# Performance work log

Measured on AMD Instinct MI355X. Metric: run time of the kernel, lower is better.

The kernel has to match this reference:

```python
import jax, jax.numpy as jnp
import numpy as np

B, T, C, H = 16, 2048, 192, 64

def setup_inputs() -> dict:
    key = jax.random.key(0)
    k1, k2, k3, k4 = jax.random.split(key, 4)
    x = jax.random.normal(k1, (B, T, C), dtype=jnp.float32)
    Wq = jax.random.normal(k2, (C, H), dtype=jnp.float32) * (C ** -0.5)
    Wk = jax.random.normal(k3, (C, H), dtype=jnp.float32) * (C ** -0.5)
    Wv = jax.random.normal(k4, (C, H), dtype=jnp.float32) * (C ** -0.5)
    return {"x": x, "Wq": Wq, "Wk": Wk, "Wv": Wv}

def reference(x, Wq, Wk, Wv):
    # One head of causal self-attention (dropout in eval mode / identity).
    q = x @ Wq                       # [B, T, H]
    k = x @ Wk                       # [B, T, H]
    v = x @ Wv                       # [B, T, H]
    scale = q.shape[-1] ** -0.5
    wei = jnp.einsum('bth,bsh->bts', q, k) * scale   # [B, T, T]
    t = wei.shape[-1]
    causal = jnp.tril(jnp.ones((t, t), dtype=bool))  # tril mask
    wei = jnp.where(causal, wei, -jnp.inf)
    wei = jax.nn.softmax(wei, axis=-1)
    out = jnp.einsum('bts,bsh->bth', wei, v)         # [B, T, H]
    return out
```

## Files before the change

### kernel.cpp

```cpp
#include <hip/hip_runtime.h>

#define B 16
#define T 2048
#define C 192
#define H 64

typedef __bf16 bf16x8 __attribute__((ext_vector_type(8)));
typedef __bf16 bf16x4 __attribute__((ext_vector_type(4)));
typedef float  f32x4  __attribute__((ext_vector_type(4)));

#define MFMA(a, b, c) __builtin_amdgcn_mfma_f32_16x16x32_bf16(a, b, c, 0, 0, 0)

#define SM_BIAS 24.0f

__global__ __launch_bounds__(512) void qkv_mfma_kernel(
    const float* __restrict__ x,
    const float* __restrict__ Wq, const float* __restrict__ Wk,
    const float* __restrict__ Wv,
    __bf16* __restrict__ qb, __bf16* __restrict__ kb, __bf16* __restrict__ vt)
{
    __shared__ __bf16 Ws[192][200];
    __shared__ __bf16 tile[128][72];

    const int tid  = threadIdx.x;
    const int w    = tid >> 6;
    const int lid  = tid & 15;
    const int quad = (tid & 63) >> 4;
    const int m0   = blockIdx.x * 128 + w * 16;

    #pragma unroll
    for (int i = 0; i < 18; i++) {
        const int p = i * 512 + tid;
        const int m = p / 3072;
        const int r = p - m * 3072;
        const int k = r >> 4;
        const int nc4 = (r & 15) << 2;
        const float* W = (m == 0) ? Wq : (m == 1) ? Wk : Wv;
        const float4 v = *(const float4*)(W + k * H + nc4);
        const int n = m * 64 + nc4;
        Ws[n + 0][k] = (__bf16)v.x;
        Ws[n + 1][k] = (__bf16)v.y;
        Ws[n + 2][k] = (__bf16)v.z;
        Ws[n + 3][k] = (__bf16)v.w;
    }

    const float* xrow = x + (size_t)(m0 + lid) * C + quad * 8;
    bf16x8 af[6];
    #pragma unroll
    for (int kc = 0; kc < 6; kc++) {
        const float4 a0 = *(const float4*)(xrow + kc * 32);
        const float4 a1 = *(const float4*)(xrow + kc * 32 + 4);
        af[kc][0] = (__bf16)a0.x; af[kc][1] = (__bf16)a0.y;
        af[kc][2] = (__bf16)a0.z; af[kc][3] = (__bf16)a0.w;
        af[kc][4] = (__bf16)a1.x; af[kc][5] = (__bf16)a1.y;
        af[kc][6] = (__bf16)a1.z; af[kc][7] = (__bf16)a1.w;
    }
    __syncthreads();

    f32x4 acc[12] = {};
    #pragma unroll
    for (int kc = 0; kc < 6; kc++)
        #pragma unroll
        for (int nt = 0; nt < 12; nt++) {
            const bf16x8 bfr =
                *(const bf16x8*)&Ws[nt * 16 + lid][kc * 32 + quad * 8];
            acc[nt] = MFMA(af[kc], bfr, acc[nt]);
        }

    #pragma unroll
    for (int nt = 0; nt < 8; nt++) {
        const int n = nt * 16 + lid;
        __bf16* dst = (n < 64) ? qb : kb;
        const int col = n & 63;
        const float scale = (n < 64) ? 0.1803368801111204f : 1.0f;
        #pragma unroll
        for (int r = 0; r < 4; r++) {
            const int row = m0 + quad * 4 + r;
            dst[(size_t)row * H + col] = (__bf16)(acc[nt][r] * scale);
        }
    }

    #pragma unroll
    for (int nt = 8; nt < 12; nt++) {
        const int col = (nt - 8) * 16 + lid;
        #pragma unroll
        for (int r = 0; r < 4; r++)
            tile[w * 16 + quad * 4 + r][col] = (__bf16)(acc[nt][r]);
    }
    __syncthreads();

    const int bb = blockIdx.x >> 4;
    const int t0 = (blockIdx.x & 15) << 7;
    #pragma unroll
    for (int it = 0; it < 2; ++it) {
        const int q   = it * 512 + tid;
        const int h   = q >> 4;
        const int tl0 = (q & 15) * 8;
        bf16x8 d;
        #pragma unroll
        for (int j = 0; j < 8; j++) d[j] = tile[tl0 + j][h];
        *(bf16x8*)(vt + ((size_t)(bb * H + h)) * T + t0 + tl0) = d;
    }
}

__global__ __launch_bounds__(512, 4) void attn_kernel(
    const __bf16* __restrict__ qb,
    const __bf16* __restrict__ kb,
    const __bf16* __restrict__ vt,
    float* __restrict__ out)
{
    __shared__ __bf16 Kb[2][2][64][72];
    __shared__ __bf16 Vb[2][2][64][68];

    const int tid  = threadIdx.x;
    const int wv   = tid >> 6;
    const int grp  = wv >> 2;
    const int w    = wv & 3;
    const int lid  = tid & 15;
    const int quad = (tid & 63) >> 4;

    const int half = blockIdx.x >> 8;
    const int rem  = blockIdx.x & 255;
    const int b    = rem & 15;
    const int pr   = rem >> 4;
    const int qt   = half ? pr : (31 - pr);
    const int nch  = qt + 1;
    const int nsteps = (nch + 1) >> 1;
    const size_t bbase = (size_t)b * T;

    const int qX = (qt << 6) + w * 16;

    const __bf16* qr = qb + (bbase + qX + lid) * H + quad * 8;
    const bf16x8 qf0 = *(const bf16x8*)(qr);
    const bf16x8 qf1 = *(const bf16x8*)(qr + 32);

    const __bf16* kgb = kb + bbase * H;
    const __bf16* vgb = vt + (size_t)b * H * T;

    const int ra = tid >> 3, ca = (tid & 7) * 8;

    auto keyof = [&](int i) {
        if (i > nch - 1) i = nch - 1;
        return i << 6;
    };

    bf16x8 kr[2], vr2[2];
    auto prefetch = [&](int s) {
        #pragma unroll
        for (int g = 0; g < 2; g++) {
            const int key0 = keyof(2 * s + g);
            kr[g]  = *(const bf16x8*)(kgb + (size_t)(key0 + ra) * H + ca);
            vr2[g] = *(const bf16x8*)(vgb + (size_t)ra * T + key0 + ca);
        }
    };

    f32x4 O[4] = {};
    float ls = 0.f;

    auto doChunk = [&](int key0, int cur) {
        const __bf16 (*Kc)[72] = Kb[cur][grp];
        const __bf16 (*Vc)[68] = Vb[cur][grp];
        bf16x8 kf[8];
        #pragma unroll
        for (int j = 0; j < 4; j++) {
            kf[2*j]   = *(const bf16x8*)&Kc[j * 16 + lid][quad * 8];
            kf[2*j+1] = *(const bf16x8*)&Kc[j * 16 + lid][32 + quad * 8];
        }
        bf16x8 bv0[4], bv1[4];
        #pragma unroll
        for (int ht = 0; ht < 4; ht++) {
            const __bf16* vr_ = &Vc[ht * 16 + lid][quad * 4];
            ((bf16x4*)&bv0[ht])[0] = *(const bf16x4*)(vr_);
            ((bf16x4*)&bv0[ht])[1] = *(const bf16x4*)(vr_ + 16);
            ((bf16x4*)&bv1[ht])[0] = *(const bf16x4*)(vr_ + 32);
            ((bf16x4*)&bv1[ht])[1] = *(const bf16x4*)(vr_ + 48);
        }
        bf16x8 af0, af1;
        const bool boundary = (key0 + 63 > qX);
        #pragma unroll
        for (int j = 0; j < 4; j++) {
            f32x4 sS = {-SM_BIAS, -SM_BIAS, -SM_BIAS, -SM_BIAS};
            sS = MFMA(kf[2*j], qf0, sS);
            sS = MFMA(kf[2*j+1], qf1, sS);
            if (boundary) {
                #pragma unroll
                for (int r = 0; r < 4; r++)
                    if (key0 + j * 16 + quad * 4 + r > qX + lid) sS[r] = -1e30f;
            }
            #pragma unroll
            for (int r = 0; r < 4; r++) {
                const float p = __builtin_amdgcn_exp2f(sS[r]);
                ls += p;
                if      (j == 0) af0[r]     = (__bf16)p;
                else if (j == 1) af0[4 + r] = (__bf16)p;
                else if (j == 2) af1[r]     = (__bf16)p;
                else             af1[4 + r] = (__bf16)p;
            }
        }
        #pragma unroll
        for (int ht = 0; ht < 4; ht++) {
            O[ht] = MFMA(af0, bv0[ht], O[ht]);
            O[ht] = MFMA(af1, bv1[ht], O[ht]);
        }
    };

    prefetch(0);
    int cur = 0;
    for (int s = 0; s < nsteps; s++) {
        *(bf16x8*)&Kb[cur][0][ra][ca] = kr[0];
        *(bf16x8*)&Kb[cur][1][ra][ca] = kr[1];
        *(bf16x8*)&Vb[cur][0][ra][ca] = vr2[0];
        *(bf16x8*)&Vb[cur][1][ra][ca] = vr2[1];
        __syncthreads();
        if (s + 1 < nsteps) prefetch(s + 1);

        const int i = 2 * s + grp;
        if (i < nch) doChunk(i << 6, cur);
        cur ^= 1;
    }

    __syncthreads();
    float* sO = (float*)&Kb[0][0][0][0];
    float* sL = (float*)&Vb[0][0][0][0];

    float l = ls;
    l += __shfl_xor(l, 16, 64);
    l += __shfl_xor(l, 32, 64);

    if (grp == 1) {
        #pragma unroll
        for (int ht = 0; ht < 4; ht++)
            #pragma unroll
            for (int r = 0; r < 4; r++)
                sO[(w * 16 + quad * 4 + r) * 64 + ht * 16 + lid] = O[ht][r];
        if ((tid & 63) < 16) sL[w * 16 + lid] = l;
    }
    __syncthreads();
    if (grp == 0) {
        l += sL[w * 16 + lid];
        #pragma unroll
        for (int ht = 0; ht < 4; ht++)
            #pragma unroll
            for (int r = 0; r < 4; r++) {
                const float Lr = __shfl(l, quad * 4 + r, 16);
                const float v = O[ht][r]
                    + sO[(w * 16 + quad * 4 + r) * 64 + ht * 16 + lid];
                out[(bbase + qX + quad * 4 + r) * H + ht * 16 + lid] = v / Lr;
            }
    }
}

extern "C" void kernel_launch(void* const* d_in, const int* in_sizes, int n_in,
                              void* d_out, int out_size, void* d_ws, size_t ws_size,
                              hipStream_t stream)
{
    const float* x  = (const float*)d_in[0];
    const float* Wq = (const float*)d_in[1];
    const float* Wk = (const float*)d_in[2];
    const float* Wv = (const float*)d_in[3];

    const size_t BTH = (size_t)B * T * H;
    __bf16* qbuf = (__bf16*)d_ws;
    __bf16* kbuf = qbuf + BTH;
    __bf16* vtb  = kbuf + BTH;
    float* outp = (float*)d_out;

    qkv_mfma_kernel<<<B * T / 128, 512, 0, stream>>>(x, Wq, Wk, Wv,
                                                     qbuf, kbuf, vtb);
    attn_kernel<<<B * T / 128 * 2, 512, 0, stream>>>(qbuf, kbuf, vtb, outp);
}
```

Measured before the change: 101.6 us.

## Pre-pack weights into MFMA fragment layout and split QKV projection across wave groups

Adds a small kernel that converts Wq/Wk/Wv to bf16 once per call and stores them in the exact per-lane MFMA B-fragment order in workspace. The projection kernel then reads weight fragments straight from global memory instead of having every block rebuild a 192x192 bf16 copy in LDS. Each block now covers 64 rows, with two wave groups each computing half of the output columns, which doubles the block count and shrinks LDS use. The cost is an extra kernel launch, and every wave now reads its weight fragments from global or L2 instead of LDS.

Measured after the change: 106.2 us. 1.05x slower.

```diff
diff --git a/kernel.cpp b/kernel.cpp
--- a/kernel.cpp
+++ b/kernel.cpp
@@ -13,36 +13,39 @@
 
 #define SM_BIAS 24.0f
 
-__global__ __launch_bounds__(512) void qkv_mfma_kernel(
+__global__ __launch_bounds__(512) void wtrans_kernel(
+    const float* __restrict__ Wq, const float* __restrict__ Wk,
+    const float* __restrict__ Wv, __bf16* __restrict__ Wf)
+{
+    const int idx  = blockIdx.x * 512 + threadIdx.x;
+    const int ntg  = idx / 384;
+    const int rem  = idx - ntg * 384;
+    const int kc   = rem >> 6;
+    const int lane = rem & 63;
+    const float* Wm = (ntg < 4) ? Wq : (ntg < 8) ? Wk : Wv;
+    const int nl = ((ntg & 3) << 4) + (lane & 15);
+    const int k0 = kc * 32 + (lane >> 4) * 8;
+    bf16x8 d;
+    #pragma unroll
+    for (int j = 0; j < 8; j++) d[j] = (__bf16)Wm[(k0 + j) * H + nl];
+    *(bf16x8*)(Wf + (size_t)idx * 8) = d;
+}
+
+__global__ __launch_bounds__(512, 4) void qkv_mfma_kernel(
     const float* __restrict__ x,
-    const float* __restrict__ Wq, const float* __restrict__ Wk,
-    const float* __restrict__ Wv,
+    const __bf16* __restrict__ Wf,
     __bf16* __restrict__ qb, __bf16* __restrict__ kb, __bf16* __restrict__ vt)
 {
-    __shared__ __bf16 Ws[192][200];
-    __shared__ __bf16 tile[128][72];
+    __shared__ __bf16 tile[64][72];
 
     const int tid  = threadIdx.x;
     const int w    = tid >> 6;
+    const int wg   = w >> 2;
+    const int wr   = w & 3;
+    const int lane = tid & 63;
     const int lid  = tid & 15;
-    const int quad = (tid & 63) >> 4;
-    const int m0   = blockIdx.x * 128 + w * 16;
-
-    #pragma unroll
-    for (int i = 0; i < 18; i++) {
-        const int p = i * 512 + tid;
-        const int m = p / 3072;
-        const int r = p - m * 3072;
-        const int k = r >> 4;
-        const int nc4 = (r & 15) << 2;
-        const float* W = (m == 0) ? Wq : (m == 1) ? Wk : Wv;
-        const float4 v = *(const float4*)(W + k * H + nc4);
-        const int n = m * 64 + nc4;
-        Ws[n + 0][k] = (__bf16)v.x;
-        Ws[n + 1][k] = (__bf16)v.y;
-        Ws[n + 2][k] = (__bf16)v.z;
-        Ws[n + 3][k] = (__bf16)v.w;
-    }
+    const int quad = lane >> 4;
+    const int m0   = blockIdx.x * 64 + wr * 16;
 
     const float* xrow = x + (size_t)(m0 + lid) * C + quad * 8;
     bf16x8 af[6];
@@ -55,47 +58,45 @@
         af[kc][4] = (__bf16)a1.x; af[kc][5] = (__bf16)a1.y;
         af[kc][6] = (__bf16)a1.z; af[kc][7] = (__bf16)a1.w;
     }
+
+    f32x4 acc[6] = {};
+    #pragma unroll
+    for (int kc = 0; kc < 6; kc++)
+        #pragma unroll
+        for (int nt = 0; nt < 6; nt++) {
+            const int ntg = wg * 6 + nt;
+            const bf16x8 bfr = *(const bf16x8*)(
+                Wf + (((size_t)(ntg * 6 + kc)) * 64 + lane) * 8);
+            acc[nt] = MFMA(af[kc], bfr, acc[nt]);
+        }
+
+    #pragma unroll
+    for (int nt = 0; nt < 6; nt++) {
+        const int ntg = wg * 6 + nt;
+        const int n = ntg * 16 + lid;
+        if (ntg < 8) {
+            __bf16* dst = (ntg < 4) ? qb : kb;
+            const int col = n & 63;
+            const float scale = (ntg < 4) ? 0.1803368801111204f : 1.0f;
+            #pragma unroll
+            for (int r = 0; r < 4; r++) {
+                const int row = m0 + quad * 4 + r;
+                dst[(size_t)row * H + col] = (__bf16)(acc[nt][r] * scale);
+            }
+        } else {
+            const int col = n - 128;
+            #pragma unroll
+            for (int r = 0; r < 4; r++)
+                tile[wr * 16 + quad * 4 + r][col] = (__bf16)(acc[nt][r]);
+        }
+    }
     __syncthreads();
 
-    f32x4 acc[12] = {};
-    #pragma unroll
-    for (int kc = 0; kc < 6; kc++)
-        #pragma unroll
-        for (int nt = 0; nt < 12; nt++) {
-            const bf16x8 bfr =
-                *(const bf16x8*)&Ws[nt * 16 + lid][kc * 32 + quad * 8];
-            acc[nt] = MFMA(af[kc], bfr, acc[nt]);
-        }
-
-    #pragma unroll
-    for (int nt = 0; nt < 8; nt++) {
-        const int n = nt * 16 + lid;
-        __bf16* dst = (n < 64) ? qb : kb;
-        const int col = n & 63;
-        const float scale = (n < 64) ? 0.1803368801111204f : 1.0f;
-        #pragma unroll
-        for (int r = 0; r < 4; r++) {
-            const int row = m0 + quad * 4 + r;
-            dst[(size_t)row * H + col] = (__bf16)(acc[nt][r] * scale);
-        }
-    }
-
-    #pragma unroll
-    for (int nt = 8; nt < 12; nt++) {
-        const int col = (nt - 8) * 16 + lid;
-        #pragma unroll
-        for (int r = 0; r < 4; r++)
-            tile[w * 16 + quad * 4 + r][col] = (__bf16)(acc[nt][r]);
-    }
-    __syncthreads();
-
-    const int bb = blockIdx.x >> 4;
-    const int t0 = (blockIdx.x & 15) << 7;
-    #pragma unroll
-    for (int it = 0; it < 2; ++it) {
-        const int q   = it * 512 + tid;
-        const int h   = q >> 4;
-        const int tl0 = (q & 15) * 8;
+    const int bb = blockIdx.x >> 5;
+    const int t0 = (blockIdx.x & 31) << 6;
+    {
+        const int h   = tid >> 3;
+        const int tl0 = (tid & 7) * 8;
         bf16x8 d;
         #pragma unroll
         for (int j = 0; j < 8; j++) d[j] = tile[tl0 + j][h];
@@ -263,9 +264,10 @@
     __bf16* qbuf = (__bf16*)d_ws;
     __bf16* kbuf = qbuf + BTH;
     __bf16* vtb  = kbuf + BTH;
+    __bf16* Wfb  = vtb + BTH;
     float* outp = (float*)d_out;
 
-    qkv_mfma_kernel<<<B * T / 128, 512, 0, stream>>>(x, Wq, Wk, Wv,
-                                                     qbuf, kbuf, vtb);
+    wtrans_kernel<<<9, 512, 0, stream>>>(Wq, Wk, Wv, Wfb);
+    qkv_mfma_kernel<<<B * T / 64, 512, 0, stream>>>(x, Wfb, qbuf, kbuf, vtb);
     attn_kernel<<<B * T / 128 * 2, 512, 0, stream>>>(qbuf, kbuf, vtb, outp);
 }
```

## Issue next-tile prefetch before LDS stores with ping-pong registers and MFMA priority

Applied to the files above, without the earlier changes.

The global-memory prefetch for step s+1 is now issued before the current tile is written to LDS and before the barrier. Alternating register sets (ping-pong A/B with a manually unrolled loop) make this possible, giving the loads longer to complete. MFMA sections are wrapped in s_setprio to favour matrix issue across waves. The row-sum accumulator becomes a 4-wide vector to break a serial add dependency. The extra register sets raise VGPR pressure, which could hurt occupancy under launch_bounds(512,4).

New measurement: 132.3 us. 30.3% more time.

```diff
diff --git a/kernel.cpp b/kernel.cpp
--- a/kernel.cpp
+++ b/kernel.cpp
@@ -144,18 +144,17 @@
         return i << 6;
     };
 
-    bf16x8 kr[2], vr2[2];
-    auto prefetch = [&](int s) {
+    auto prefetchInto = [&](bf16x8 (&kr)[2], bf16x8 (&vr)[2], int s) {
         #pragma unroll
         for (int g = 0; g < 2; g++) {
             const int key0 = keyof(2 * s + g);
-            kr[g]  = *(const bf16x8*)(kgb + (size_t)(key0 + ra) * H + ca);
-            vr2[g] = *(const bf16x8*)(vgb + (size_t)ra * T + key0 + ca);
+            kr[g] = *(const bf16x8*)(kgb + (size_t)(key0 + ra) * H + ca);
+            vr[g] = *(const bf16x8*)(vgb + (size_t)ra * T + key0 + ca);
         }
     };
 
     f32x4 O[4] = {};
-    float ls = 0.f;
+    f32x4 lsv = {0.f, 0.f, 0.f, 0.f};
 
     auto doChunk = [&](int key0, int cur) {
         const __bf16 (*Kc)[72] = Kb[cur][grp];
@@ -180,8 +179,10 @@
         #pragma unroll
         for (int j = 0; j < 4; j++) {
             f32x4 sS = {-SM_BIAS, -SM_BIAS, -SM_BIAS, -SM_BIAS};
+            __builtin_amdgcn_s_setprio(1);
             sS = MFMA(kf[2*j], qf0, sS);
             sS = MFMA(kf[2*j+1], qf1, sS);
+            __builtin_amdgcn_s_setprio(0);
             if (boundary) {
                 #pragma unroll
                 for (int r = 0; r < 4; r++)
@@ -190,40 +191,50 @@
             #pragma unroll
             for (int r = 0; r < 4; r++) {
                 const float p = __builtin_amdgcn_exp2f(sS[r]);
-                ls += p;
+                lsv[r] += p;
                 if      (j == 0) af0[r]     = (__bf16)p;
                 else if (j == 1) af0[4 + r] = (__bf16)p;
                 else if (j == 2) af1[r]     = (__bf16)p;
                 else             af1[4 + r] = (__bf16)p;
             }
         }
+        __builtin_amdgcn_s_setprio(1);
         #pragma unroll
         for (int ht = 0; ht < 4; ht++) {
             O[ht] = MFMA(af0, bv0[ht], O[ht]);
             O[ht] = MFMA(af1, bv1[ht], O[ht]);
         }
-    };
-
-    prefetch(0);
+        __builtin_amdgcn_s_setprio(0);
+    };
+
+    bf16x8 krA[2], vrA[2], krB[2], vrB[2];
     int cur = 0;
-    for (int s = 0; s < nsteps; s++) {
-        *(bf16x8*)&Kb[cur][0][ra][ca] = kr[0];
-        *(bf16x8*)&Kb[cur][1][ra][ca] = kr[1];
-        *(bf16x8*)&Vb[cur][0][ra][ca] = vr2[0];
-        *(bf16x8*)&Vb[cur][1][ra][ca] = vr2[1];
+
+    auto step = [&](int s, bf16x8 (&krC)[2], bf16x8 (&vrC)[2],
+                    bf16x8 (&krN)[2], bf16x8 (&vrN)[2]) {
+        if (s + 1 < nsteps) prefetchInto(krN, vrN, s + 1);
+        *(bf16x8*)&Kb[cur][0][ra][ca] = krC[0];
+        *(bf16x8*)&Kb[cur][1][ra][ca] = krC[1];
+        *(bf16x8*)&Vb[cur][0][ra][ca] = vrC[0];
+        *(bf16x8*)&Vb[cur][1][ra][ca] = vrC[1];
         __syncthreads();
-        if (s + 1 < nsteps) prefetch(s + 1);
-
         const int i = 2 * s + grp;
         if (i < nch) doChunk(i << 6, cur);
         cur ^= 1;
+    };
+
+    prefetchInto(krA, vrA, 0);
+    int s = 0;
+    while (s < nsteps) {
+        step(s, krA, vrA, krB, vrB); s++;
+        if (s < nsteps) { step(s, krB, vrB, krA, vrA); s++; }
     }
 
     __syncthreads();
     float* sO = (float*)&Kb[0][0][0][0];
     float* sL = (float*)&Vb[0][0][0][0];
 
-    float l = ls;
+    float l = lsv[0] + lsv[1] + lsv[2] + lsv[3];
     l += __shfl_xor(l, 16, 64);
     l += __shfl_xor(l, 32, 64);
 
```
